# Kernel optimization log

Hardware: AMD Instinct MI355X
Metric: run time of the kernel (lower is better)

Reference implementation:

```python
import jax, jax.numpy as jnp
import numpy as np

B, T, INP_DIM, H = 32, 2000, 4, 512
TC = 0.01  # t_const


def setup_inputs() -> dict:
    key = jax.random.key(0)
    ks = jax.random.split(key, 10)
    inp = jax.random.normal(ks[0], (B, T, INP_DIM), dtype=jnp.float32)
    hn = jax.random.uniform(ks[1], (1, B, 2 * H), dtype=jnp.float32)
    x = jnp.zeros((1, B, 2 * H), jnp.float32)
    inhib_stim = jnp.zeros((B, T, 2 * H), jnp.float32)
    u = lambda k, s, hi: jax.random.uniform(k, s, jnp.float32, 0.0, hi)
    str2str_w = u(ks[2], (H, H), 0.01)
    alm2alm_w = u(ks[3], (H, H), 0.01)
    alm2str_w = u(ks[4], (H, H), 0.01)
    str2alm_w = u(ks[5], (H, H), 0.01)
    inp_weight = u(ks[6], (INP_DIM, 2 * H), 0.01)
    sparse_mask = (jax.random.uniform(ks[7], (H, H)) < 0.1).astype(jnp.float32)
    str2str_fixed = u(ks[8], (H, H), 0.001) * sparse_mask
    str2str_mask = jnp.zeros((H, H), jnp.float32)
    n_inhib = int(0.3 * H)
    alm2str_mask = jnp.concatenate(
        [jnp.ones((H, H - n_inhib), jnp.float32), jnp.zeros((H, n_inhib), jnp.float32)], axis=1)
    alm2alm_sign = jnp.concatenate(
        [jnp.ones((H - n_inhib,), jnp.float32), -jnp.ones((n_inhib,), jnp.float32)])
    str_d1_mask = jnp.concatenate([jnp.ones((H,), jnp.float32), jnp.zeros((H,), jnp.float32)])
    return dict(inp=inp, hn=hn, x=x, inhib_stim=inhib_stim,
                str2str_w=str2str_w, alm2alm_w=alm2alm_w, alm2str_w=alm2str_w,
                str2alm_w=str2alm_w, inp_weight=inp_weight,
                str2str_fixed=str2str_fixed, str2str_mask=str2str_mask,
                alm2str_mask=alm2str_mask, alm2alm_sign=alm2alm_sign,
                str_d1_mask=str_d1_mask)


def _build_wrec(str2str_w, alm2alm_w, alm2str_w, str2alm_w,
                str2str_fixed, str2str_mask, alm2str_mask, alm2alm_sign):
    clip01 = lambda w: jnp.clip(w, 1e-15, 1.0)  # F.hardtanh(w, 1e-15, 1)
    str2str = -(str2str_mask * clip01(str2str_w) + str2str_fixed)      # @ (-I)
    alm2alm = clip01(alm2alm_w) * alm2alm_sign[None, :]                # @ diag(sign)
    alm2str = alm2str_mask * clip01(alm2str_w)
    str2alm = clip01(str2alm_w)
    W_str = jnp.concatenate([str2str, alm2str], axis=1)
    W_alm = jnp.concatenate([str2alm, alm2alm], axis=1)
    return jnp.concatenate([W_str, W_alm], axis=0)  # [2H, 2H]


def reference(inp, hn, x, inhib_stim, str2str_w, alm2alm_w, alm2str_w, str2alm_w,
              inp_weight, str2str_fixed, str2str_mask, alm2str_mask,
              alm2alm_sign, str_d1_mask):
    W_rec = _build_wrec(str2str_w, alm2alm_w, alm2str_w, str2alm_w,
                        str2str_fixed, str2str_mask, alm2str_mask, alm2alm_sign)
    # input drive precomputed for all steps: [B, T, 2H] (noise=False path)
    drive = jnp.einsum('bti,ih->bth', inp, inp_weight) * str_d1_mask + inhib_stim
    h0 = hn[0]  # [B, 2H]

    def step(h, d_t):
        h_new = jax.nn.relu(h + TC * (-h + h @ W_rec.T + d_t))
        return h_new, h_new

    _, hs = jax.lax.scan(step, h0, jnp.swapaxes(drive, 0, 1))  # [T, B, 2H]
    rnn_out = jnp.swapaxes(hs, 0, 1)                            # [B, T, 2H]
    x_out = jnp.broadcast_to(x[0][:, None, :], rnn_out.shape)   # x never updated
    hn_last = rnn_out[:, -1, :][None]
    x_last = x_out[:, -1, :][None]
    return (hn_last, rnn_out, x_last, x_out)
```

## Files before the change

kernel.cpp:

```cpp
#include <hip/hip_runtime.h>
#include <stdint.h>

#define H2      1024
#define TSTEPS  2000
#define TC_C    0.01f

#define NGROUPS   8
#define WG_PER_G  8
#define BPG       4
#define ROWS_WG   128
#define NTHR      512
#define NBLOCKS   (NGROUPS * WG_PER_G)
#define NLAUNCH   254

#define OFF_RNN   32768
#define OFF_XL    (32768 + 65536000)
#define OFF_XO    (OFF_XL + 32768)

#define FLAG_BASE 32768
#define STOP_OFF  (FLAG_BASE + 192)

#define HPAD 520

typedef __attribute__((ext_vector_type(8))) short bf16x8;
typedef __attribute__((ext_vector_type(4))) float f32x4;

#define AT_LOAD(p)     __hip_atomic_load((p), __ATOMIC_RELAXED, __HIP_MEMORY_SCOPE_AGENT)
#define AT_STORE(p, v) __hip_atomic_store((p), (v), __ATOMIC_RELAXED, __HIP_MEMORY_SCOPE_AGENT)

__device__ __forceinline__ float clip01(float w) {
  return fminf(fmaxf(w, 1e-15f), 1.0f);
}
__device__ __forceinline__ uint32_t f2bf(float x) {
  uint32_t u = __float_as_uint(x);
  return ((u + 0x7fffu + ((u >> 16) & 1u)) >> 16) & 0xffffu;
}

__global__ void stralm_init_kernel(const float* __restrict__ hn,
                                   const float* __restrict__ x,
                                   float* __restrict__ out,
                                   float* __restrict__ ws) {
  const int tid = blockIdx.x * 256 + threadIdx.x;
  const int b  = tid >> 11;
  const int r  = tid & 2047;
  const int jq = (r & 255) * 4;
  const int t0 = (r >> 8) * 250;
  const float4 xv = *(const float4*)(x + b * H2 + jq);
  float* xo = out + OFF_XO;
  for (int i = 0; i < 250; ++i) {
    const int t = t0 + i;
    *(float4*)(xo + (size_t)(b * TSTEPS + t) * H2 + jq) = xv;
  }
  uint32_t* buf32 = (uint32_t*)ws;
  if (tid < 16384) {
    const float2 hv = *(const float2*)(hn + tid * 2);
    buf32[tid] = f2bf(hv.x) | (f2bf(hv.y) << 16);
  }
  if (tid < 8192)
    *(float4*)(out + OFF_XL + tid * 4) = *(const float4*)(x + tid * 4);
  if (tid < 256) ((int*)ws)[FLAG_BASE + tid] = 0;
}

__global__ __launch_bounds__(NTHR, 1) void stralm_rnn_kernel(
    const float* __restrict__ inp,
    const float* __restrict__ hn,
    const float* __restrict__ inhib,
    const float* __restrict__ ss_w, const float* __restrict__ a2a_w,
    const float* __restrict__ a2s_w, const float* __restrict__ s2a_w,
    const float* __restrict__ iw,
    const float* __restrict__ ss_fix, const float* __restrict__ ss_mask,
    const float* __restrict__ a2s_mask, const float* __restrict__ sign_v,
    const float* __restrict__ d1mask,
    float* __restrict__ out, float* __restrict__ ws) {
  const int tid = threadIdx.x;
  int* stop = (int*)ws + STOP_OFF;

  if (blockIdx.x >= NBLOCKS) {
    float a = (float)tid * 1.0e-6f + 1.0f;
    const float bm = 1.0000001f, cm = 0.9999999f;
    for (;;) {
#pragma unroll 16
      for (int i = 0; i < 1024; ++i) a = __builtin_fmaf(a, bm, cm);
      asm volatile("" :: "v"(a));
      if (AT_LOAD(stop) != 0) break;
    }
    return;
  }

  __shared__ __align__(16) uint32_t smem[8256];

  const int g   = blockIdx.x & 7;
  const int wg  = blockIdx.x >> 3;
  const int r0  = wg * ROWS_WG;
  const int l   = tid & 63;
  const int wv  = tid >> 6;

  uint32_t* buf32 = (uint32_t*)ws;
  int*      flags = (int*)ws + FLAG_BASE + g * 16;

  bf16x8 afr[32];
  {
    unsigned short* wstage = (unsigned short*)smem;
    for (int mt = 0; mt < 8; ++mt) {
      __syncthreads();
      for (int i = 0; i < 32; ++i) {
        const int idx = i * NTHR + tid;
        const int jt  = idx >> 10;
        const int k   = idx & 1023;
        const int jg  = r0 + mt * 16 + jt;
        const int jq  = jg & 511;
        float w;
        if (jg < 512) {
          if (k < 512)
            w = -(ss_mask[jq * 512 + k] * clip01(ss_w[jq * 512 + k]) +
                  ss_fix[jq * 512 + k]);
          else {
            const int kk = k - 512;
            w = a2s_mask[jq * 512 + kk] * clip01(a2s_w[jq * 512 + kk]);
          }
        } else {
          if (k < 512)
            w = clip01(s2a_w[jq * 512 + k]);
          else {
            const int kk = k - 512;
            w = clip01(a2a_w[jq * 512 + kk]) * sign_v[kk];
          }
        }
        wstage[jt * 1032 + k] = (unsigned short)f2bf(w);
      }
      __syncthreads();
      if (wv == mt) {
#pragma unroll
        for (int kt = 0; kt < 32; ++kt)
          afr[kt] = *(const bf16x8*)&wstage[(l & 15) * 1032 + kt * 32 +
                                            (l >> 4) * 8];
      }
    }
  }
  __syncthreads();

  uint32_t* h_lds = smem;

  const int  n    = l & 15;
  const bool act  = (n < 4);
  const int  h4   = l >> 4;
  const int  bg   = g * BPG + (act ? n : 0);
  const int  grow = r0 + wv * 16 + h4 * 4;
  float4 iwr0 = {}, iwr1 = {}, iwr2 = {}, iwr3 = {}, dmr = {}, hold = {};
  float4 inh_cur = {}, ip_cur = {};
  if (act) {
    iwr0 = *(const float4*)(iw + 0 * H2 + grow);
    iwr1 = *(const float4*)(iw + 1 * H2 + grow);
    iwr2 = *(const float4*)(iw + 2 * H2 + grow);
    iwr3 = *(const float4*)(iw + 3 * H2 + grow);
    dmr  = *(const float4*)(d1mask + grow);
    hold = *(const float4*)(hn + bg * H2 + grow);
    inh_cur = *(const float4*)(inhib + (size_t)bg * TSTEPS * H2 + grow);
    ip_cur  = *(const float4*)(inp + bg * (TSTEPS * 4));
  }
  const int bb = l & 3;

  for (int t = 0; t < TSTEPS; ++t) {
    const int p = t & 1;
    if (tid < WG_PER_G) {
      while (AT_LOAD(flags + tid) < t) __builtin_amdgcn_s_sleep(1);
    }
    __syncthreads();

    {
      const uint64_t* src64 = (const uint64_t*)(buf32 + p * 16384 + g * 2048);
      const uint64_t v0 = __hip_atomic_load(src64 + tid, __ATOMIC_RELAXED,
                                            __HIP_MEMORY_SCOPE_AGENT);
      const uint64_t v1 = __hip_atomic_load(src64 + 512 + tid, __ATOMIC_RELAXED,
                                            __HIP_MEMORY_SCOPE_AGENT);
      uint32_t* hbuf = h_lds + p * (4 * HPAD);
      const int e0 = 2 * tid;
      const int e1 = 1024 + 2 * tid;
      *(uint64_t*)(hbuf + (e0 >> 9) * HPAD + (e0 & 511)) = v0;
      *(uint64_t*)(hbuf + (e1 >> 9) * HPAD + (e1 & 511)) = v1;
    }
    __syncthreads();

    const unsigned short* hsb =
        (const unsigned short*)(h_lds + p * (4 * HPAD)) + bb * (2 * HPAD) +
        h4 * 8;
    f32x4 a0 = {0.f, 0.f, 0.f, 0.f}, a1 = a0, a2 = a0, a3 = a0;
#pragma unroll
    for (int j = 0; j < 8; ++j) {
      const bf16x8 b0 = *(const bf16x8*)&hsb[(j)      * 32];
      const bf16x8 b1 = *(const bf16x8*)&hsb[(8 + j)  * 32];
      const bf16x8 b2 = *(const bf16x8*)&hsb[(16 + j) * 32];
      const bf16x8 b3 = *(const bf16x8*)&hsb[(24 + j) * 32];
      a0 = __builtin_amdgcn_mfma_f32_16x16x32_bf16(afr[j],      b0, a0, 0, 0, 0);
      a1 = __builtin_amdgcn_mfma_f32_16x16x32_bf16(afr[8 + j],  b1, a1, 0, 0, 0);
      a2 = __builtin_amdgcn_mfma_f32_16x16x32_bf16(afr[16 + j], b2, a2, 0, 0, 0);
      a3 = __builtin_amdgcn_mfma_f32_16x16x32_bf16(afr[24 + j], b3, a3, 0, 0, 0);
    }
    const f32x4 acc = (a0 + a1) + (a2 + a3);

    float h0 = 0.f, h1 = 0.f, h2 = 0.f, h3 = 0.f;
    if (act) {
      const float d0 = dmr.x * (iwr0.x * ip_cur.x + iwr1.x * ip_cur.y +
                                iwr2.x * ip_cur.z + iwr3.x * ip_cur.w) + inh_cur.x;
      const float d1 = dmr.y * (iwr0.y * ip_cur.x + iwr1.y * ip_cur.y +
                                iwr2.y * ip_cur.z + iwr3.y * ip_cur.w) + inh_cur.y;
      const float d2 = dmr.z * (iwr0.z * ip_cur.x + iwr1.z * ip_cur.y +
                                iwr2.z * ip_cur.z + iwr3.z * ip_cur.w) + inh_cur.z;
      const float d3 = dmr.w * (iwr0.w * ip_cur.x + iwr1.w * ip_cur.y +
                                iwr2.w * ip_cur.z + iwr3.w * ip_cur.w) + inh_cur.w;
      h0 = fmaxf(0.f, (1.f - TC_C) * hold.x + TC_C * (acc[0] + d0));
      h1 = fmaxf(0.f, (1.f - TC_C) * hold.y + TC_C * (acc[1] + d1));
      h2 = fmaxf(0.f, (1.f - TC_C) * hold.z + TC_C * (acc[2] + d2));
      h3 = fmaxf(0.f, (1.f - TC_C) * hold.w + TC_C * (acc[3] + d3));
      hold = (float4){h0, h1, h2, h3};
      const uint64_t pk2 = (uint64_t)(f2bf(h0) | (f2bf(h1) << 16)) |
                           ((uint64_t)(f2bf(h2) | (f2bf(h3) << 16)) << 32);
      uint64_t* ep = (uint64_t*)(buf32 + (p ^ 1) * 16384 + bg * 512) +
                     (grow >> 2);
      __hip_atomic_store(ep, pk2, __ATOMIC_RELAXED, __HIP_MEMORY_SCOPE_AGENT);
    }
    asm volatile("s_waitcnt vmcnt(0)" ::: "memory");
    __syncthreads();
    if (tid == 0)
      AT_STORE(flags + wg, t + 1);
    if (act) {
      const f32x4 hv4 = {h0, h1, h2, h3};
      __builtin_nontemporal_store(
          hv4, (f32x4*)(out + OFF_RNN + (size_t)bg * (TSTEPS * H2) +
                        (size_t)t * H2 + grow));
      if (t == TSTEPS - 1)
        *(float4*)(out + bg * H2 + grow) = (float4){h0, h1, h2, h3};
      const int tn = (t < TSTEPS - 1) ? t + 1 : TSTEPS - 1;
      inh_cur = *(const float4*)(inhib + ((size_t)bg * TSTEPS + tn) * H2 + grow);
      ip_cur  = *(const float4*)(inp + bg * (TSTEPS * 4) + tn * 4);
    }
  }
  if (tid == 0) AT_STORE(stop, 1);
}

extern "C" void kernel_launch(void* const* d_in, const int* in_sizes, int n_in,
                              void* d_out, int out_size, void* d_ws,
                              size_t ws_size, hipStream_t stream) {
  const float* inp      = (const float*)d_in[0];
  const float* hn       = (const float*)d_in[1];
  const float* x        = (const float*)d_in[2];
  const float* inhib    = (const float*)d_in[3];
  const float* ss_w     = (const float*)d_in[4];
  const float* a2a_w    = (const float*)d_in[5];
  const float* a2s_w    = (const float*)d_in[6];
  const float* s2a_w    = (const float*)d_in[7];
  const float* iw       = (const float*)d_in[8];
  const float* ss_fix   = (const float*)d_in[9];
  const float* ss_mask  = (const float*)d_in[10];
  const float* a2s_mask = (const float*)d_in[11];
  const float* sign_v   = (const float*)d_in[12];
  const float* d1mask   = (const float*)d_in[13];
  float* out = (float*)d_out;
  float* ws  = (float*)d_ws;

  hipLaunchKernelGGL(stralm_init_kernel, dim3(256), dim3(256), 0, stream,
                     hn, x, out, ws);
  hipLaunchKernelGGL(stralm_rnn_kernel, dim3(NLAUNCH), dim3(NTHR), 0, stream,
                     inp, hn, inhib, ss_w, a2a_w, a2s_w, s2a_w, iw, ss_fix,
                     ss_mask, a2s_mask, sign_v, d1mask, out, ws);
}
```

Baseline: 4.804 ms.

## Replace flag polling with per-consumer flag lines and wave-level arrival counter

Each workgroup now gets its own flag cache line, and producers write their step counter into every consumer's line. An LDS atomic counter lets the last wave to finish signal, instead of a full workgroup barrier before the flag store. The spin-wait no longer sleeps, and the extra busy-spinning filler blocks are removed, so only the 64 working blocks launch. This targets per-step synchronization latency, at the cost of more flag stores and of losing whatever clock or occupancy effect the filler blocks provided.

```diff
diff --git a/kernel.cpp b/kernel.cpp
--- a/kernel.cpp
+++ b/kernel.cpp
@@ -11,14 +11,12 @@
 #define ROWS_WG   128
 #define NTHR      512
 #define NBLOCKS   (NGROUPS * WG_PER_G)
-#define NLAUNCH   254
 
 #define OFF_RNN   32768
 #define OFF_XL    (32768 + 65536000)
 #define OFF_XO    (OFF_XL + 32768)
 
 #define FLAG_BASE 32768
-#define STOP_OFF  (FLAG_BASE + 192)
 
 #define HPAD 520
 
@@ -58,7 +56,7 @@
   }
   if (tid < 8192)
     *(float4*)(out + OFF_XL + tid * 4) = *(const float4*)(x + tid * 4);
-  if (tid < 256) ((int*)ws)[FLAG_BASE + tid] = 0;
+  if (tid < 1024) ((int*)ws)[FLAG_BASE + tid] = 0;
 }
 
 __global__ __launch_bounds__(NTHR, 1) void stralm_rnn_kernel(
@@ -72,31 +70,18 @@
     const float* __restrict__ a2s_mask, const float* __restrict__ sign_v,
     const float* __restrict__ d1mask,
     float* __restrict__ out, float* __restrict__ ws) {
+  __shared__ __align__(16) uint32_t smem[8256];
+
   const int tid = threadIdx.x;
-  int* stop = (int*)ws + STOP_OFF;
-
-  if (blockIdx.x >= NBLOCKS) {
-    float a = (float)tid * 1.0e-6f + 1.0f;
-    const float bm = 1.0000001f, cm = 0.9999999f;
-    for (;;) {
-#pragma unroll 16
-      for (int i = 0; i < 1024; ++i) a = __builtin_fmaf(a, bm, cm);
-      asm volatile("" :: "v"(a));
-      if (AT_LOAD(stop) != 0) break;
-    }
-    return;
-  }
-
-  __shared__ __align__(16) uint32_t smem[8256];
-
   const int g   = blockIdx.x & 7;
   const int wg  = blockIdx.x >> 3;
   const int r0  = wg * ROWS_WG;
   const int l   = tid & 63;
   const int wv  = tid >> 6;
 
-  uint32_t* buf32 = (uint32_t*)ws;
-  int*      flags = (int*)ws + FLAG_BASE + g * 16;
+  uint32_t* buf32    = (uint32_t*)ws;
+  int*      flagbase = (int*)ws + FLAG_BASE;
+  int*      myline   = flagbase + (g * 8 + wg) * 16;
 
   bf16x8 afr[32];
   {
@@ -138,6 +123,9 @@
     }
   }
   __syncthreads();
+  int* wcnt = (int*)&smem[8192];
+  if (tid == 0) *wcnt = 0;
+  __syncthreads();
 
   uint32_t* h_lds = smem;
 
@@ -163,7 +151,7 @@
   for (int t = 0; t < TSTEPS; ++t) {
     const int p = t & 1;
     if (tid < WG_PER_G) {
-      while (AT_LOAD(flags + tid) < t) __builtin_amdgcn_s_sleep(1);
+      while (AT_LOAD(myline + tid) < t) {}
     }
     __syncthreads();
 
@@ -220,9 +208,13 @@
       __hip_atomic_store(ep, pk2, __ATOMIC_RELAXED, __HIP_MEMORY_SCOPE_AGENT);
     }
     asm volatile("s_waitcnt vmcnt(0)" ::: "memory");
-    __syncthreads();
-    if (tid == 0)
-      AT_STORE(flags + wg, t + 1);
+    int oldv = 0;
+    if (l == 0)
+      oldv = __hip_atomic_fetch_add(wcnt, 1, __ATOMIC_ACQ_REL,
+                                    __HIP_MEMORY_SCOPE_WORKGROUP);
+    oldv = __shfl(oldv, 0);
+    if (oldv == 8 * t + 7 && l < 8)
+      AT_STORE(flagbase + (g * 8 + l) * 16 + wg, t + 1);
     if (act) {
       const f32x4 hv4 = {h0, h1, h2, h3};
       __builtin_nontemporal_store(
@@ -235,7 +227,6 @@
       ip_cur  = *(const float4*)(inp + bg * (TSTEPS * 4) + tn * 4);
     }
   }
-  if (tid == 0) AT_STORE(stop, 1);
 }
 
 extern "C" void kernel_launch(void* const* d_in, const int* in_sizes, int n_in,
@@ -260,7 +251,7 @@
 
   hipLaunchKernelGGL(stralm_init_kernel, dim3(256), dim3(256), 0, stream,
                      hn, x, out, ws);
-  hipLaunchKernelGGL(stralm_rnn_kernel, dim3(NLAUNCH), dim3(NTHR), 0, stream,
+  hipLaunchKernelGGL(stralm_rnn_kernel, dim3(NBLOCKS), dim3(NTHR), 0, stream,
                      inp, hn, inhib, ss_w, a2a_w, a2s_w, s2a_w, iw, ss_fix,
                      ss_mask, a2s_mask, sign_v, d1mask, out, ws);
 }
```

New measurement: 5.365 ms. 11.7% more time.
